# Kernel optimization log

Measured on AMD Instinct MI355X. Metric: run time of the kernel, lower is better.

## Reference

```python
import jax, jax.numpy as jnp
import numpy as np

DIM = 1024
H = 16          # query heads
HKV = 4         # kv heads
HD = DIM // H   # head_dim = 64
B = 8           # equal-length docs
S = 1024        # tokens per doc
N = B * S       # total tokens
ROPE_BASE = 10000.0


def _rms_norm(x, scale):
    eps = jnp.asarray(jnp.finfo(x.dtype).eps, x.dtype)
    inv = jax.lax.rsqrt(jnp.mean(x * x, axis=-1, keepdims=True) + eps)
    return x * inv * scale


def _rope(x, cos, sin):
    # x: [N, h, HD]; cos/sin: [N, 1, HD//2]
    half = x.shape[-1] // 2
    x1, x2 = x[..., :half], x[..., half:]
    return jnp.concatenate((x1 * cos + x2 * sin, -x1 * sin + x2 * cos), axis=-1)


def setup_inputs() -> dict:
    key = jax.random.key(0)
    ks = jax.random.split(key, 8)
    x = jax.random.normal(ks[0], (N, DIM), dtype=jnp.float32)
    Wq = jax.random.normal(ks[1], (DIM, DIM), dtype=jnp.float32) * (DIM ** -0.5)
    Wk = jax.random.normal(ks[2], (HKV * HD, DIM), dtype=jnp.float32) * (DIM ** -0.5)
    Wv = jax.random.normal(ks[3], (HKV * HD, DIM), dtype=jnp.float32) * (DIM ** -0.5)
    Wproj = jax.random.normal(ks[4], (DIM, DIM), dtype=jnp.float32) * (DIM ** -0.5)
    q_gain = jnp.full((H,), 1.0, dtype=jnp.float32)
    q_scale = jnp.asarray(1.0, dtype=jnp.float32)  # q RMSNorm scale
    k_scale = jnp.asarray(1.0, dtype=jnp.float32)  # k RMSNorm scale
    # rotary tables per Rotary.prepare_positions (positions reset per doc)
    cu_seqlens = jnp.arange(B + 1, dtype=jnp.int32) * S
    positions = jnp.tile(jnp.arange(S, dtype=jnp.float32), B)  # [N]
    inv_freq = 1.0 / (ROPE_BASE ** (jnp.arange(0, HD, 2, dtype=jnp.float32) / HD))
    freqs = positions[:, None] * inv_freq[None, :]  # [N, HD//2]
    rotary_cos = jnp.cos(freqs)[:, None, :]
    rotary_sin = jnp.sin(freqs)[:, None, :]
    return {
        "x": x, "Wq": Wq, "Wk": Wk, "Wv": Wv, "Wproj": Wproj,
        "q_gain": q_gain, "q_scale": q_scale, "k_scale": k_scale,
        "rotary_cos": rotary_cos, "rotary_sin": rotary_sin,
        "cu_seqlens": cu_seqlens, "max_doc_len": S,
    }


def reference(x, Wq, Wk, Wv, Wproj, q_gain, q_scale, k_scale,
              rotary_cos, rotary_sin, cu_seqlens, max_doc_len):
    n_tokens, dim = x.shape
    q = (x @ Wq.T).reshape(n_tokens, H, HD)
    k = (x @ Wk.T).reshape(n_tokens, HKV, HD)
    v = (x @ Wv.T).reshape(n_tokens, HKV, HD)
    q = _rms_norm(q, q_scale)
    k = _rms_norm(k, k_scale)
    q = _rope(q, rotary_cos, rotary_sin)
    k = _rope(k, rotary_cos, rotary_sin)
    q = q * q_gain[None, :, None]
    # equal-length docs -> [B, S, h, HD]; GQA: repeat kv heads
    rep = H // HKV
    qb = q.reshape(B, S, H, HD)
    kb = jnp.repeat(k.reshape(B, S, HKV, HD), rep, axis=2)
    vb = jnp.repeat(v.reshape(B, S, HKV, HD), rep, axis=2)
    scale = HD ** -0.5
    scores = jnp.einsum('bqhd,bkhd->bhqk', qb, kb) * scale  # [B,H,S,S]
    causal = jnp.tril(jnp.ones((S, S), dtype=bool))
    scores = jnp.where(causal[None, None], scores, jnp.asarray(-jnp.inf, scores.dtype))
    attn = jax.nn.softmax(scores, axis=-1)
    y = jnp.einsum('bhqk,bkhd->bqhd', attn, vb).reshape(n_tokens, dim)
    return y @ Wproj.T
```

## Files before the change

### kernel.cpp

```cpp
#include <hip/hip_runtime.h>
#include <hip/hip_bf16.h>


typedef __bf16 bf16x8 __attribute__((ext_vector_type(8)));
typedef float f32x4 __attribute__((ext_vector_type(4)));

__device__ __forceinline__ void async16(const void* g, void* l) {
  __builtin_amdgcn_global_load_lds((const __attribute__((address_space(1))) void*)g,
                                   (__attribute__((address_space(3))) void*)l, 16, 0, 0);
}

__device__ __forceinline__ unsigned short f2bfu(float x) {
  __hip_bfloat16 h = __float2bfloat16(x);
  return __builtin_bit_cast(unsigned short, h);
}

__global__ __launch_bounds__(256) void castall(
    const float4* __restrict__ x, const float4* __restrict__ Wq,
    const float4* __restrict__ Wk, const float4* __restrict__ Wv,
    const float4* __restrict__ Wp,
    ushort4* __restrict__ xb, ushort4* __restrict__ w1b, ushort4* __restrict__ wpb) {
  int i = blockIdx.x * 256 + threadIdx.x;
  const float4* src;
  ushort4* dst;
  if (i < 2097152)      { src = x + i;             dst = xb + i; }
  else if (i < 2359296) { src = Wq + (i - 2097152); dst = w1b + (i - 2097152); }
  else if (i < 2424832) { src = Wk + (i - 2359296); dst = w1b + (i - 2097152); }
  else if (i < 2490368) { src = Wv + (i - 2424832); dst = w1b + (i - 2097152); }
  else                  { src = Wp + (i - 2490368); dst = wpb + (i - 2490368); }
  float4 v = *src;
  ushort4 o;
  o.x = f2bfu(v.x); o.y = f2bfu(v.y); o.z = f2bfu(v.z); o.w = f2bfu(v.w);
  *dst = o;
}

__global__ __launch_bounds__(256, 3) void gemm_qkv(
    const __hip_bfloat16* __restrict__ A,
    const __hip_bfloat16* __restrict__ Bm,
    const float* __restrict__ cosb, const float* __restrict__ sinb,
    const float* __restrict__ qgain, const float* __restrict__ qscale,
    const float* __restrict__ kscale,
    __hip_bfloat16* __restrict__ Qo,
    __hip_bfloat16* __restrict__ Ko,
    __hip_bfloat16* __restrict__ Vo)
{
  __shared__ __align__(16) unsigned short As[128 * 32];
  __shared__ __align__(16) unsigned short Bs[128 * 32];
  const int tid = threadIdx.x;
  const int wave = tid >> 6, lane = tid & 63;
  const int quad = lane >> 4, l15 = lane & 15;
  const int bn = blockIdx.x, bm = blockIdx.y;
  const int wm = (wave >> 1) * 64, wn = (wave & 1) * 64;
  const int srow = lane >> 2, scol = (lane & 3) * 8;
  const int K = 1024;

  f32x4 acc[4][4] = {};

  const __hip_bfloat16* Ab = A + (size_t)bm * 128 * K;
  const __hip_bfloat16* Bb = Bm + (size_t)bn * 128 * K;

  for (int kt = 0; kt < K; kt += 32) {
    __syncthreads();
#pragma unroll
    for (int c = 0; c < 2; c++) {
      const int ch = wave * 2 + c;
      async16(Ab + (size_t)(ch * 16 + srow) * K + kt + scol, &As[ch * 512]);
      async16(Bb + (size_t)(ch * 16 + srow) * K + kt + scol, &Bs[ch * 512]);
    }
    __syncthreads();
    bf16x8 af[4], bfr[4];
#pragma unroll
    for (int mt = 0; mt < 4; mt++)
      af[mt] = *(const bf16x8*)&As[(wm + mt * 16 + l15) * 32 + quad * 8];
#pragma unroll
    for (int nt = 0; nt < 4; nt++)
      bfr[nt] = *(const bf16x8*)&Bs[(wn + nt * 16 + l15) * 32 + quad * 8];
#pragma unroll
    for (int mt = 0; mt < 4; mt++)
#pragma unroll
      for (int nt = 0; nt < 4; nt++)
        acc[mt][nt] = __builtin_amdgcn_mfma_f32_16x16x32_bf16(af[mt], bfr[nt], acc[mt][nt], 0, 0, 0);
  }

  const int hg = bn * 2 + (wn >> 6);
  const int tokbase = bm * 128 + wm;

  if (hg >= 20) {
    const int hv = hg - 20;
#pragma unroll
    for (int mt = 0; mt < 4; mt++)
#pragma unroll
      for (int r = 0; r < 4; r++) {
        const int tok = tokbase + mt * 16 + quad * 4 + r;
#pragma unroll
        for (int nt = 0; nt < 4; nt++)
          Vo[(size_t)tok * 256 + hv * 64 + nt * 16 + l15] = __float2bfloat16(acc[mt][nt][r]);
      }
  } else {
    const bool isq = hg < 16;
    const float scale = isq ? qscale[0] : kscale[0];
    const float gain = isq ? qgain[hg] : 1.0f;
    const float sg = scale * gain;
#pragma unroll
    for (int mt = 0; mt < 4; mt++) {
      float inv[4];
#pragma unroll
      for (int r = 0; r < 4; r++) {
        float ss = acc[mt][0][r] * acc[mt][0][r] + acc[mt][1][r] * acc[mt][1][r] +
                   acc[mt][2][r] * acc[mt][2][r] + acc[mt][3][r] * acc[mt][3][r];
#pragma unroll
        for (int off = 1; off < 16; off <<= 1) ss += __shfl_xor(ss, off);
        inv[r] = rsqrtf(ss * (1.0f / 64.0f) + 1.1920929e-07f) * sg;
      }
#pragma unroll
      for (int r = 0; r < 4; r++) {
        const int tok = tokbase + mt * 16 + quad * 4 + r;
        const float c0 = cosb[tok * 32 + l15], c1 = cosb[tok * 32 + 16 + l15];
        const float s0 = sinb[tok * 32 + l15], s1 = sinb[tok * 32 + 16 + l15];
        const float v0 = acc[mt][0][r] * inv[r];
        const float v1 = acc[mt][1][r] * inv[r];
        const float v2 = acc[mt][2][r] * inv[r];
        const float v3 = acc[mt][3][r] * inv[r];
        const float o0 = v0 * c0 + v2 * s0;
        const float o1 = v1 * c1 + v3 * s1;
        const float o2 = -v0 * s0 + v2 * c0;
        const float o3 = -v1 * s1 + v3 * c1;
        __hip_bfloat16* base = isq ? (Qo + (size_t)tok * 1024 + hg * 64)
                                   : (Ko + (size_t)tok * 256 + (hg - 16) * 64);
        base[l15]      = __float2bfloat16(o0);
        base[16 + l15] = __float2bfloat16(o1);
        base[32 + l15] = __float2bfloat16(o2);
        base[48 + l15] = __float2bfloat16(o3);
      }
    }
  }
}

__global__ __launch_bounds__(256, 4) void gemm_p(
    const __hip_bfloat16* __restrict__ A,
    const __hip_bfloat16* __restrict__ Bm,
    float* __restrict__ C)
{
  __shared__ __align__(16) unsigned short As[128 * 32];
  __shared__ __align__(16) unsigned short Bs[64 * 32];
  const int tid = threadIdx.x;
  const int wave = tid >> 6, lane = tid & 63;
  const int quad = lane >> 4, l15 = lane & 15;
  const int bn = blockIdx.x, bm = blockIdx.y;
  const int wm = wave * 32;
  const int srow = lane >> 2, scol = (lane & 3) * 8;
  const int K = 1024;

  f32x4 acc[2][4] = {};

  const __hip_bfloat16* Ab = A + (size_t)bm * 128 * K;
  const __hip_bfloat16* Bb = Bm + (size_t)bn * 64 * K;

  for (int kt = 0; kt < K; kt += 32) {
    __syncthreads();
#pragma unroll
    for (int c = 0; c < 2; c++) {
      const int ch = wave * 2 + c;
      async16(Ab + (size_t)(ch * 16 + srow) * K + kt + scol, &As[ch * 512]);
    }
    async16(Bb + (size_t)(wave * 16 + srow) * K + kt + scol, &Bs[wave * 512]);
    __syncthreads();
    bf16x8 af[2], bfr[4];
#pragma unroll
    for (int mt = 0; mt < 2; mt++)
      af[mt] = *(const bf16x8*)&As[(wm + mt * 16 + l15) * 32 + quad * 8];
#pragma unroll
    for (int nt = 0; nt < 4; nt++)
      bfr[nt] = *(const bf16x8*)&Bs[(nt * 16 + l15) * 32 + quad * 8];
#pragma unroll
    for (int mt = 0; mt < 2; mt++)
#pragma unroll
      for (int nt = 0; nt < 4; nt++)
        acc[mt][nt] = __builtin_amdgcn_mfma_f32_16x16x32_bf16(af[mt], bfr[nt], acc[mt][nt], 0, 0, 0);
  }

#pragma unroll
  for (int mt = 0; mt < 2; mt++)
#pragma unroll
    for (int nt = 0; nt < 4; nt++)
#pragma unroll
      for (int r = 0; r < 4; r++) {
        const int row = bm * 128 + wm + mt * 16 + quad * 4 + r;
        const int col = bn * 64 + nt * 16 + l15;
        C[(size_t)row * 1024 + col] = acc[mt][nt][r];
      }
}

__global__ __launch_bounds__(256) void vtrans(const unsigned short* __restrict__ vkb,
                                              unsigned short* __restrict__ Vt) {
  __shared__ unsigned short t[64][65];
  const int st = blockIdx.x, kvh = blockIdx.y, b = blockIdx.z;
  const int tid = threadIdx.x;
  const int s0 = st * 64;
#pragma unroll
  for (int i = 0; i < 16; i++) {
    const int idx = tid + i * 256;
    const int sl = idx >> 6, d = idx & 63;
    t[sl][d] = vkb[(size_t)(b * 1024 + s0 + sl) * 256 + kvh * 64 + d];
  }
  __syncthreads();
#pragma unroll
  for (int i = 0; i < 16; i++) {
    const int idx = tid + i * 256;
    const int d = idx >> 6, sl = idx & 63;
    Vt[((size_t)(b * 4 + kvh) * 64 + d) * 1024 + s0 + sl] = t[sl][d];
  }
}

__global__ __launch_bounds__(512, 4) void attn(
    const __hip_bfloat16* __restrict__ Q,
    const __hip_bfloat16* __restrict__ Kk,
    const __hip_bfloat16* __restrict__ Vt,
    __hip_bfloat16* __restrict__ Y)
{
  __shared__ __align__(16) unsigned short Kb[2][4096];
  __shared__ __align__(16) unsigned short Vb[2][4096];
  __shared__ __align__(16) unsigned short Pm[8][32 * 72];
  __shared__ float Lsh[8][32];

  const int xx = blockIdx.x;
  const int qt = (xx & 1) ? (xx >> 1) : (15 - (xx >> 1));
  const int kvh = blockIdx.y, b = blockIdx.z;
  const int tid = threadIdx.x;
  const int wave = tid >> 6, lane = tid & 63;
  const int quad = lane >> 4, l15 = lane & 15;
  const int h = kvh * 4 + (wave >> 1);
  const int m0 = (wave & 1) * 32;
  const int tok0 = b * 1024 + qt * 64;

  const int srow = lane >> 2;
  const int scol = (lane & 3) * 8;

  bf16x8 qf[2][2];
#pragma unroll
  for (int mt = 0; mt < 2; mt++)
#pragma unroll
    for (int kc = 0; kc < 2; kc++)
      qf[mt][kc] = *(const bf16x8*)(Q + (size_t)(tok0 + m0 + mt * 16 + l15) * 1024 +
                                    h * 64 + kc * 32 + quad * 8);

  auto issue = [&](int kt, unsigned short* Ks, unsigned short* Vs) {
#pragma unroll
    for (int c = 0; c < 2; c++) {
      const int ch = wave * 2 + c;
      const int v = ch >> 3;
      const int ch8 = ch & 7;
      const int kc = ch8 >> 2, grp = ch8 & 3;
      if (v == 0)
        async16(Kk + (size_t)(b * 1024 + kt * 64 + grp * 16 + srow) * 256 + kvh * 64 + kc * 32 + scol,
                Ks + kc * 2048 + grp * 512 + lane * 8);
      else
        async16(Vt + ((size_t)((b * 4 + kvh) * 64 + grp * 16 + srow)) * 1024 + kt * 64 + kc * 32 + scol,
                Vs + kc * 2048 + grp * 512 + lane * 8);
    }
  };

  issue(0, Kb[0], Vb[0]);

  f32x4 of[2][4] = {};
  float lsum[2] = {0.0f, 0.0f};
  const float scl2 = 0.125f * 1.44269504089f;
  unsigned short* Pw = Pm[wave];

  for (int kt = 0; kt <= qt; kt++) {
    __syncthreads();
    if (kt < qt) issue(kt + 1, Kb[(kt + 1) & 1], Vb[(kt + 1) & 1]);
    const unsigned short* Ks = Kb[kt & 1];
    const unsigned short* Vs = Vb[kt & 1];

    f32x4 sf[4][2] = {};
#pragma unroll
    for (int kc = 0; kc < 2; kc++) {
#pragma unroll
      for (int kk = 0; kk < 4; kk++) {
        const bf16x8 kf = *(const bf16x8*)&Ks[kc * 2048 + (kk * 16 + l15) * 32 + quad * 8];
#pragma unroll
        for (int mt = 0; mt < 2; mt++)
          sf[kk][mt] = __builtin_amdgcn_mfma_f32_16x16x32_bf16(kf, qf[mt][kc], sf[kk][mt], 0, 0, 0);
      }
    }

    const bool diag = (kt == qt);
#pragma unroll
    for (int mt = 0; mt < 2; mt++) {
#pragma unroll
      for (int kk = 0; kk < 4; kk++) {
        ushort4 pk;
        unsigned short* pp = (unsigned short*)&pk;
#pragma unroll
        for (int r = 0; r < 4; r++) {
          float p;
          if (diag && (kk * 16 + quad * 4 + r) > (m0 + mt * 16 + l15)) {
            p = 0.0f;
          } else {
            p = __builtin_amdgcn_exp2f(sf[kk][mt][r] * scl2);
          }
          lsum[mt] += p;
          pp[r] = f2bfu(p);
        }
        *(ushort4*)&Pw[(mt * 16 + l15) * 72 + kk * 16 + quad * 4] = pk;
      }
    }

    asm volatile("s_waitcnt lgkmcnt(0)" ::: "memory");

#pragma unroll
    for (int kc = 0; kc < 2; kc++) {
#pragma unroll
      for (int mt = 0; mt < 2; mt++) {
        const bf16x8 ap = *(const bf16x8*)&Pw[(mt * 16 + l15) * 72 + kc * 32 + quad * 8];
#pragma unroll
        for (int dt = 0; dt < 4; dt++) {
          const bf16x8 bv = *(const bf16x8*)&Vs[kc * 2048 + (dt * 16 + l15) * 32 + quad * 8];
          of[mt][dt] = __builtin_amdgcn_mfma_f32_16x16x32_bf16(ap, bv, of[mt][dt], 0, 0, 0);
        }
      }
    }
  }

#pragma unroll
  for (int mt = 0; mt < 2; mt++) {
    float l = lsum[mt];
    l += __shfl_xor(l, 16);
    l += __shfl_xor(l, 32);
    Lsh[wave][mt * 16 + l15] = l;
  }
  asm volatile("s_waitcnt lgkmcnt(0)" ::: "memory");

#pragma unroll
  for (int mt = 0; mt < 2; mt++)
#pragma unroll
    for (int r = 0; r < 4; r++) {
      const float rcp = 1.0f / Lsh[wave][mt * 16 + quad * 4 + r];
      const int row = tok0 + m0 + mt * 16 + quad * 4 + r;
#pragma unroll
      for (int dt = 0; dt < 4; dt++)
        Y[(size_t)row * 1024 + h * 64 + dt * 16 + l15] = __float2bfloat16(of[mt][dt][r] * rcp);
    }
}

extern "C" void kernel_launch(void* const* d_in, const int* in_sizes, int n_in,
                              void* d_out, int out_size, void* d_ws, size_t ws_size,
                              hipStream_t stream) {
  const float* x      = (const float*)d_in[0];
  const float* Wq     = (const float*)d_in[1];
  const float* Wk     = (const float*)d_in[2];
  const float* Wv     = (const float*)d_in[3];
  const float* Wp     = (const float*)d_in[4];
  const float* qgain  = (const float*)d_in[5];
  const float* qscale = (const float*)d_in[6];
  const float* kscale = (const float*)d_in[7];
  const float* cosb   = (const float*)d_in[8];
  const float* sinb   = (const float*)d_in[9];
  float* out = (float*)d_out;
  char* ws = (char*)d_ws;

  __hip_bfloat16* xb  = (__hip_bfloat16*)(ws);
  __hip_bfloat16* w1b = (__hip_bfloat16*)(ws + 16777216);
  __hip_bfloat16* wpb = (__hip_bfloat16*)(ws + 19922944);
  __hip_bfloat16* qb  = (__hip_bfloat16*)(ws + 22020096);
  __hip_bfloat16* kb  = (__hip_bfloat16*)(ws + 38797312);
  __hip_bfloat16* vkb = (__hip_bfloat16*)(ws + 42991616);
  __hip_bfloat16* vtb = (__hip_bfloat16*)(ws + 47185920);
  __hip_bfloat16* yb  = (__hip_bfloat16*)(ws + 51380224);

  castall<<<10752, 256, 0, stream>>>((const float4*)x, (const float4*)Wq, (const float4*)Wk,
                                     (const float4*)Wv, (const float4*)Wp,
                                     (ushort4*)xb, (ushort4*)w1b, (ushort4*)wpb);

  gemm_qkv<<<dim3(12, 64), 256, 0, stream>>>(xb, w1b, cosb, sinb, qgain, qscale, kscale,
                                             qb, kb, vkb);

  vtrans<<<dim3(16, 4, 8), 256, 0, stream>>>((const unsigned short*)vkb, (unsigned short*)vtb);

  attn<<<dim3(16, 4, 8), 512, 0, stream>>>(qb, kb, vtb, yb);

  gemm_p<<<dim3(16, 64), 256, 0, stream>>>(yb, wpb, out);
}
```

Measured before the change: 220.3 us.

## Fuse V transpose into QKV GEMM epilogue and split attention into 32-row query blocks

The QKV GEMM epilogue now writes V directly in transposed [b,kvh,d,s] layout with packed 4-element stores, which removes the separate vtrans kernel and its extra read/write pass. The attention kernel is restructured to 256-thread blocks that each cover 32 query rows across 4 heads, launched as twice as many blocks, so causal work is finer-grained and load-balanced. Each block now reloads K/V tiles for its own half of the query tile, which raises global/L2 traffic. The V stores are strided across rows, which may be less coalesced.

```diff
diff --git a/kernel.cpp b/kernel.cpp
--- a/kernel.cpp
+++ b/kernel.cpp
@@ -42,7 +42,7 @@
     const float* __restrict__ kscale,
     __hip_bfloat16* __restrict__ Qo,
     __hip_bfloat16* __restrict__ Ko,
-    __hip_bfloat16* __restrict__ Vo)
+    __hip_bfloat16* __restrict__ Vt)
 {
   __shared__ __align__(16) unsigned short As[128 * 32];
   __shared__ __align__(16) unsigned short Bs[128 * 32];
@@ -87,15 +87,21 @@
 
   if (hg >= 20) {
     const int hv = hg - 20;
-#pragma unroll
-    for (int mt = 0; mt < 4; mt++)
-#pragma unroll
-      for (int r = 0; r < 4; r++) {
-        const int tok = tokbase + mt * 16 + quad * 4 + r;
-#pragma unroll
-        for (int nt = 0; nt < 4; nt++)
-          Vo[(size_t)tok * 256 + hv * 64 + nt * 16 + l15] = __float2bfloat16(acc[mt][nt][r]);
-      }
+    const int bb = tokbase >> 10;
+    const int sbase = (tokbase & 1023) + quad * 4;
+    unsigned short* vt = (unsigned short*)Vt;
+#pragma unroll
+    for (int nt = 0; nt < 4; nt++) {
+      const size_t rowoff = ((size_t)((bb * 4 + hv) * 64 + nt * 16 + l15)) * 1024;
+#pragma unroll
+      for (int mt = 0; mt < 4; mt++) {
+        ushort4 pk;
+        unsigned short* pp = (unsigned short*)&pk;
+#pragma unroll
+        for (int r = 0; r < 4; r++) pp[r] = f2bfu(acc[mt][nt][r]);
+        *(ushort4*)&vt[rowoff + sbase + mt * 16] = pk;
+      }
+    }
   } else {
     const bool isq = hg < 16;
     const float scale = isq ? qscale[0] : kscale[0];
@@ -191,28 +197,7 @@
       }
 }
 
-__global__ __launch_bounds__(256) void vtrans(const unsigned short* __restrict__ vkb,
-                                              unsigned short* __restrict__ Vt) {
-  __shared__ unsigned short t[64][65];
-  const int st = blockIdx.x, kvh = blockIdx.y, b = blockIdx.z;
-  const int tid = threadIdx.x;
-  const int s0 = st * 64;
-#pragma unroll
-  for (int i = 0; i < 16; i++) {
-    const int idx = tid + i * 256;
-    const int sl = idx >> 6, d = idx & 63;
-    t[sl][d] = vkb[(size_t)(b * 1024 + s0 + sl) * 256 + kvh * 64 + d];
-  }
-  __syncthreads();
-#pragma unroll
-  for (int i = 0; i < 16; i++) {
-    const int idx = tid + i * 256;
-    const int d = idx >> 6, sl = idx & 63;
-    Vt[((size_t)(b * 4 + kvh) * 64 + d) * 1024 + s0 + sl] = t[sl][d];
-  }
-}
-
-__global__ __launch_bounds__(512, 4) void attn(
+__global__ __launch_bounds__(256, 3) void attn(
     const __hip_bfloat16* __restrict__ Q,
     const __hip_bfloat16* __restrict__ Kk,
     const __hip_bfloat16* __restrict__ Vt,
@@ -220,18 +205,19 @@
 {
   __shared__ __align__(16) unsigned short Kb[2][4096];
   __shared__ __align__(16) unsigned short Vb[2][4096];
-  __shared__ __align__(16) unsigned short Pm[8][32 * 72];
-  __shared__ float Lsh[8][32];
+  __shared__ __align__(16) unsigned short Pm[4][32 * 72];
+  __shared__ float Lsh[4][32];
 
   const int xx = blockIdx.x;
-  const int qt = (xx & 1) ? (xx >> 1) : (15 - (xx >> 1));
+  const int qh = (xx & 1) ? (xx >> 1) : (31 - (xx >> 1));
   const int kvh = blockIdx.y, b = blockIdx.z;
   const int tid = threadIdx.x;
   const int wave = tid >> 6, lane = tid & 63;
   const int quad = lane >> 4, l15 = lane & 15;
-  const int h = kvh * 4 + (wave >> 1);
-  const int m0 = (wave & 1) * 32;
-  const int tok0 = b * 1024 + qt * 64;
+  const int h = kvh * 4 + wave;
+  const int tok0 = b * 1024 + qh * 32;
+  const int m0 = (qh & 1) * 32;
+  const int nkt = (qh >> 1) + 1;
 
   const int srow = lane >> 2;
   const int scol = (lane & 3) * 8;
@@ -241,13 +227,13 @@
   for (int mt = 0; mt < 2; mt++)
 #pragma unroll
     for (int kc = 0; kc < 2; kc++)
-      qf[mt][kc] = *(const bf16x8*)(Q + (size_t)(tok0 + m0 + mt * 16 + l15) * 1024 +
+      qf[mt][kc] = *(const bf16x8*)(Q + (size_t)(tok0 + mt * 16 + l15) * 1024 +
                                     h * 64 + kc * 32 + quad * 8);
 
   auto issue = [&](int kt, unsigned short* Ks, unsigned short* Vs) {
 #pragma unroll
-    for (int c = 0; c < 2; c++) {
-      const int ch = wave * 2 + c;
+    for (int c = 0; c < 4; c++) {
+      const int ch = wave * 4 + c;
       const int v = ch >> 3;
       const int ch8 = ch & 7;
       const int kc = ch8 >> 2, grp = ch8 & 3;
@@ -267,9 +253,9 @@
   const float scl2 = 0.125f * 1.44269504089f;
   unsigned short* Pw = Pm[wave];
 
-  for (int kt = 0; kt <= qt; kt++) {
-    __syncthreads();
-    if (kt < qt) issue(kt + 1, Kb[(kt + 1) & 1], Vb[(kt + 1) & 1]);
+  for (int kt = 0; kt < nkt; kt++) {
+    __syncthreads();
+    if (kt + 1 < nkt) issue(kt + 1, Kb[(kt + 1) & 1], Vb[(kt + 1) & 1]);
     const unsigned short* Ks = Kb[kt & 1];
     const unsigned short* Vs = Vb[kt & 1];
 
@@ -285,7 +271,7 @@
       }
     }
 
-    const bool diag = (kt == qt);
+    const bool diag = (kt == (qh >> 1));
 #pragma unroll
     for (int mt = 0; mt < 2; mt++) {
 #pragma unroll
@@ -337,7 +323,7 @@
 #pragma unroll
     for (int r = 0; r < 4; r++) {
       const float rcp = 1.0f / Lsh[wave][mt * 16 + quad * 4 + r];
-      const int row = tok0 + m0 + mt * 16 + quad * 4 + r;
+      const int row = tok0 + mt * 16 + quad * 4 + r;
 #pragma unroll
       for (int dt = 0; dt < 4; dt++)
         Y[(size_t)row * 1024 + h * 64 + dt * 16 + l15] = __float2bfloat16(of[mt][dt][r] * rcp);
@@ -365,20 +351,17 @@
   __hip_bfloat16* wpb = (__hip_bfloat16*)(ws + 19922944);
   __hip_bfloat16* qb  = (__hip_bfloat16*)(ws + 22020096);
   __hip_bfloat16* kb  = (__hip_bfloat16*)(ws + 38797312);
-  __hip_bfloat16* vkb = (__hip_bfloat16*)(ws + 42991616);
-  __hip_bfloat16* vtb = (__hip_bfloat16*)(ws + 47185920);
-  __hip_bfloat16* yb  = (__hip_bfloat16*)(ws + 51380224);
+  __hip_bfloat16* vtb = (__hip_bfloat16*)(ws + 42991616);
+  __hip_bfloat16* yb  = (__hip_bfloat16*)(ws + 47185920);
 
   castall<<<10752, 256, 0, stream>>>((const float4*)x, (const float4*)Wq, (const float4*)Wk,
                                      (const float4*)Wv, (const float4*)Wp,
                                      (ushort4*)xb, (ushort4*)w1b, (ushort4*)wpb);
 
   gemm_qkv<<<dim3(12, 64), 256, 0, stream>>>(xb, w1b, cosb, sinb, qgain, qscale, kscale,
-                                             qb, kb, vkb);
-
-  vtrans<<<dim3(16, 4, 8), 256, 0, stream>>>((const unsigned short*)vkb, (unsigned short*)vtb);
-
-  attn<<<dim3(16, 4, 8), 512, 0, stream>>>(qb, kb, vtb, yb);
+                                             qb, kb, vtb);
+
+  attn<<<dim3(32, 4, 8), 256, 0, stream>>>(qb, kb, vtb, yb);
 
   gemm_p<<<dim3(16, 64), 256, 0, stream>>>(yb, wpb, out);
 }
```

Result: slower. 225.4 us (+2.3%).
